# Kernel optimization log

Hardware: AMD Instinct MI355X
Metric: run time of the kernel (lower is better)

The kernel has to match this reference:

```python
import jax, jax.numpy as jnp
import numpy as np

N = 4096

def _backsub(rel_bounds):
    # rel_bounds: list; first entry is ((n,1),(n,1)) input bounds, rest are
    # (out, in+1) relative-bound matrices. Returns exact abs bounds (n,1).
    cur_lb, cur_ub = rel_bounds[-1]
    for prev_lb, prev_ub in reversed(rel_bounds[:-1]):
        bias_row = jnp.zeros((1, prev_lb.shape[-1]), prev_lb.dtype).at[0, -1].set(1.0)
        plb = jnp.concatenate([prev_lb, bias_row], axis=0)
        pub = jnp.concatenate([prev_ub, bias_row], axis=0)
        wp, wn = jax.nn.relu(cur_lb), jax.nn.relu(-cur_lb)
        new_lb = wp @ plb - wn @ pub
        wp, wn = jax.nn.relu(cur_ub), jax.nn.relu(-cur_ub)
        new_ub = wp @ pub - wn @ plb
        cur_lb, cur_ub = new_lb, new_ub
    return cur_lb, cur_ub


def setup_inputs() -> dict:
    key = jax.random.key(0)
    k = jax.random.split(key, 7)
    base = jax.random.normal(k[0], (N, 1), jnp.float32)
    eps = 0.1
    lb0 = base - eps
    ub0 = base + eps
    scale = 0.02  # keep bound magnitudes realistic through the matmul chain
    W1_lb = jax.random.normal(k[1], (N, N + 1), jnp.float32) * scale
    W1_ub = W1_lb + jnp.abs(jax.random.normal(k[2], (N, N + 1), jnp.float32)) * 0.001
    W2_lb = jax.random.normal(k[3], (N, N + 1), jnp.float32) * scale
    W2_ub = W2_lb + jnp.abs(jax.random.normal(k[4], (N, N + 1), jnp.float32)) * 0.001
    alphas = jax.random.uniform(k[5], (N,), jnp.float32)
    return {"lb0": lb0, "ub0": ub0, "W1_lb": W1_lb, "W1_ub": W1_ub,
            "W2_lb": W2_lb, "W2_ub": W2_ub, "alphas": alphas}


def reference(lb0, ub0, W1_lb, W1_ub, W2_lb, W2_ub, alphas):
    prev_lb, prev_ub = _backsub([(lb0, ub0), (W1_lb, W1_ub), (W2_lb, W2_ub)])  # (N,1)
    lb_s = prev_lb[:, 0]
    ub_s = prev_ub[:, 0]
    n = lb_s.shape[0]
    dt = prev_lb.dtype

    alpha = jnp.clip(alphas, 0.0, 1.0)
    alpha = jnp.where(lb_s > 0.0, jnp.ones((), dt), alpha)
    alpha = jnp.where(ub_s <= 0.0, jnp.zeros((), dt), alpha)
    current_lb = jnp.concatenate([jnp.diag(alpha), jnp.zeros((n, 1), dt)], axis=1)

    feps = jnp.finfo(dt).eps
    slope_ub = prev_ub / (prev_ub - prev_lb + feps)          # (N,1)
    slope_ub = jnp.where(prev_lb > 0.0, jnp.ones((), dt), slope_ub)
    slope_ub = jnp.where(prev_ub < 0.0, jnp.zeros((), dt), slope_ub)
    bias_ub = -prev_lb * slope_ub
    bias_ub = jnp.where((prev_lb > 0.0) | (prev_ub < 0.0), jnp.zeros((), dt), bias_ub)
    current_ub = jnp.concatenate([jnp.diag(slope_ub[:, 0]), bias_ub], axis=1)

    # stacked rel_bound appended by the layer: [0]=lower, [1]=upper, each (N, N+1)
    return jnp.stack([current_lb, current_ub])
```

## Files before the change

### kernel.cpp

```cpp
#include <hip/hip_runtime.h>
#include <float.h>

#define N4K 4096
#define NP1 4097

typedef __attribute__((ext_vector_type(4))) float f32x4;
typedef __attribute__((ext_vector_type(16))) float f32x16;
typedef __attribute__((ext_vector_type(8))) short bf16x8;

__device__ __forceinline__ unsigned short f2bf(float x) {
    union { float f; unsigned int u; } v; v.f = x;
    unsigned int r = v.u + 0x7FFFu + ((v.u >> 16) & 1u);
    return (unsigned short)(r >> 16);
}

__device__ __forceinline__ void gload_lds16(const void* g, void* l) {
    __builtin_amdgcn_global_load_lds(
        (const __attribute__((address_space(1))) unsigned int*)g,
        (__attribute__((address_space(3))) unsigned int*)l,
        16, 0, 0);
}

__device__ __forceinline__ void bar() {
    asm volatile("" ::: "memory");
    __builtin_amdgcn_s_barrier();
    asm volatile("" ::: "memory");
}

__global__ __launch_bounds__(256) void prep_A2(const float* __restrict__ W2lb,
                                               const float* __restrict__ W2ub,
                                               const float* __restrict__ mb,
                                               const float* __restrict__ db,
                                               unsigned short* __restrict__ Abf,
                                               float* __restrict__ bias_part) {
    int b = blockIdx.x;
    int chain = b >> 12, i = b & 4095;
    const float* row = (chain ? W2ub : W2lb) + (long long)i * NP1;
    unsigned short* abf_row = Abf + ((long long)chain << 24) + (long long)i * N4K;
    float s = chain ? 1.f : -1.f;
    float part = 0.f;
#pragma unroll 4
    for (int p = 0; p < 16; ++p) {
        int k = threadIdx.x + p * 256;
        float wv = row[k];
        abf_row[k] = f2bf(wv);
        part += wv * mb[k] + s * db[k] * fabsf(wv);
    }
    __shared__ float red[4];
#pragma unroll
    for (int off = 32; off; off >>= 1) part += __shfl_down(part, off);
    if ((threadIdx.x & 63) == 0) red[threadIdx.x >> 6] = part;
    __syncthreads();
    if (threadIdx.x == 0)
        bias_part[b] = red[0] + red[1] + red[2] + red[3] + row[4096];
}

__global__ __launch_bounds__(256) void prep_B(const float* __restrict__ W1lb,
                                              const float* __restrict__ W1ub,
                                              unsigned short* __restrict__ Bmt,
                                              unsigned short* __restrict__ Bdt) {
    __shared__ unsigned short Lm[64 * 65];
    __shared__ unsigned short Ld[64 * 65];
    int j0 = blockIdx.x * 64, k0 = blockIdx.y * 64;
    int t = threadIdx.x;
    int jj = t & 63, kkb = t >> 6;
#pragma unroll 4
    for (int p = 0; p < 16; ++p) {
        int kk = kkb + p * 4;
        long long off = (long long)(k0 + kk) * NP1 + j0 + jj;
        float l = W1lb[off], u = W1ub[off];
        Lm[kk * 65 + jj] = f2bf(0.5f * (l + u));
        Ld[kk * 65 + jj] = f2bf(0.5f * (u - l));
    }
    __syncthreads();
#pragma unroll
    for (int p = 0; p < 2; ++p) {
        int jl = p * 32 + (t >> 3);
        int kl = (t & 7) * 8;
        bf16x8 vm, vd;
#pragma unroll
        for (int i = 0; i < 8; ++i) {
            vm[i] = (short)Lm[(kl + i) * 65 + jl];
            vd[i] = (short)Ld[(kl + i) * 65 + jl];
        }
        *(bf16x8*)&Bmt[(long long)(j0 + jl) * N4K + k0 + kl] = vm;
        *(bf16x8*)&Bdt[(long long)(j0 + jl) * N4K + k0 + kl] = vd;
    }
}

__global__ __launch_bounds__(256) void prep_mbdb(const float* __restrict__ W1lb,
                                                 const float* __restrict__ W1ub,
                                                 float* __restrict__ mb,
                                                 float* __restrict__ db) {
    int k = blockIdx.x * 256 + threadIdx.x;
    if (k < N4K) {
        float l = W1lb[(long long)k * NP1 + 4096];
        float u = W1ub[(long long)k * NP1 + 4096];
        mb[k] = 0.5f * (l + u);
        db[k] = 0.5f * (u - l);
    }
}

__global__ __launch_bounds__(256)
void gemm_fused(const unsigned short* __restrict__ Abf,
                const unsigned short* __restrict__ Bmt,
                const unsigned short* __restrict__ Bdt,
                const float* __restrict__ lb0,
                const float* __restrict__ ub0,
                float* __restrict__ pp) {
    __shared__ unsigned short As[3][4096];
    __shared__ unsigned short Bms[3][4096];
    __shared__ unsigned short Bds[3][4096];

    int wg = blockIdx.x;
    int swz = (wg & 7) * 256 + (wg >> 3);
    int rt = swz & 63;
    int ct = swz >> 6;

    int chain = rt >> 5;
    const unsigned short* Aptr = Abf + ((long long)chain << 24) + (long long)(rt & 31) * 128 * N4K;
    const unsigned short* Bmp = Bmt + (long long)ct * 128 * N4K;
    const unsigned short* Bdp = Bdt + (long long)ct * 128 * N4K;

    int tid = threadIdx.x;
    int lane = tid & 63, w = tid >> 6;
    int wr = w >> 1, wc = w & 1;
    int la32 = lane & 31, kg = lane >> 5;

    int sr = tid >> 2;
    int sce = ((tid & 3) ^ ((sr >> 1) & 3)) << 3;
    const unsigned short* aB = Aptr + (long long)sr * N4K + sce;
    const unsigned short* mB = Bmp + (long long)sr * N4K + sce;
    const unsigned short* dB = Bdp + (long long)sr * N4K + sce;
    const long long R64 = 64LL * N4K;
    unsigned w512 = w * 512;

    f32x16 acc[2][2];
#pragma unroll
    for (int m = 0; m < 2; ++m)
#pragma unroll
        for (int n = 0; n < 2; ++n) acc[m][n] = (f32x16)(0.f);

#define STAGE(slot, koff)                                              \
    do {                                                               \
        gload_lds16(aB + (koff), &As[slot][w512]);                     \
        gload_lds16(aB + R64 + (koff), &As[slot][2048 + w512]);        \
        gload_lds16(mB + (koff), &Bms[slot][w512]);                    \
        gload_lds16(mB + R64 + (koff), &Bms[slot][2048 + w512]);       \
        gload_lds16(dB + (koff), &Bds[slot][w512]);                    \
        gload_lds16(dB + R64 + (koff), &Bds[slot][2048 + w512]);       \
    } while (0)

    STAGE(0, 0);
    STAGE(1, 32);
    asm volatile("s_waitcnt vmcnt(6)" ::: "memory");
    bar();

#define FRAG(arr, s, r, ks) \
    (*(const bf16x8*)&arr[s][(r) * 32 + (((2 * (ks) + kg) ^ (((r) >> 1) & 3)) * 8)])

    int cs = 0, st = 2;
#pragma unroll 1
    for (int t = 0; t < 128; ++t) {
        const bool pf = (t + 2 < 128);
        const long long koff = (long long)(t + 2) * 32;

        bf16x8 a[2][2], bm[2][2], bd[2][2];

#pragma unroll
        for (int m = 0; m < 2; ++m)
#pragma unroll
            for (int ks = 0; ks < 2; ++ks)
                a[m][ks] = FRAG(As, cs, wr * 64 + m * 32 + la32, ks);
#pragma unroll
        for (int n = 0; n < 2; ++n)
#pragma unroll
            for (int ks = 0; ks < 2; ++ks)
                bm[n][ks] = FRAG(Bms, cs, wc * 64 + n * 32 + la32, ks);
        if (pf) {
            gload_lds16(aB + koff, &As[st][w512]);
            gload_lds16(aB + R64 + koff, &As[st][2048 + w512]);
            gload_lds16(mB + koff, &Bms[st][w512]);
        }
        bar();
        asm volatile("s_waitcnt lgkmcnt(0)" ::: "memory");
        __builtin_amdgcn_s_setprio(1);
#pragma unroll
        for (int ks = 0; ks < 2; ++ks)
#pragma unroll
            for (int m = 0; m < 2; ++m)
#pragma unroll
                for (int n = 0; n < 2; ++n)
                    acc[m][n] = __builtin_amdgcn_mfma_f32_32x32x16_bf16(a[m][ks], bm[n][ks], acc[m][n], 0, 0, 0);
        __builtin_amdgcn_s_setprio(0);
        bar();

#pragma unroll
        for (int n = 0; n < 2; ++n)
#pragma unroll
            for (int ks = 0; ks < 2; ++ks)
                bd[n][ks] = FRAG(Bds, cs, wc * 64 + n * 32 + la32, ks);
        if (pf) {
            gload_lds16(mB + R64 + koff, &Bms[st][2048 + w512]);
            gload_lds16(dB + koff, &Bds[st][w512]);
            gload_lds16(dB + R64 + koff, &Bds[st][2048 + w512]);
        }
        bar();
        asm volatile("s_waitcnt lgkmcnt(0)" ::: "memory");
        __builtin_amdgcn_s_setprio(1);
#pragma unroll
        for (int ks = 0; ks < 2; ++ks)
#pragma unroll
            for (int m = 0; m < 2; ++m) {
                bf16x8 ax = chain ? (a[m][ks] & (short)0x7FFF) : (a[m][ks] | (short)0x8000);
#pragma unroll
                for (int n = 0; n < 2; ++n)
                    acc[m][n] = __builtin_amdgcn_mfma_f32_32x32x16_bf16(ax, bd[n][ks], acc[m][n], 0, 0, 0);
            }
        __builtin_amdgcn_s_setprio(0);

        if (pf) asm volatile("s_waitcnt vmcnt(6)" ::: "memory");
        else    asm volatile("s_waitcnt vmcnt(0)" ::: "memory");
        bar();

        cs = (cs == 2) ? 0 : cs + 1;
        st = (st == 2) ? 0 : st + 1;
    }
#undef FRAG
#undef STAGE

    float s = chain ? 1.f : -1.f;
    float rowpart[2][16];
#pragma unroll
    for (int m = 0; m < 2; ++m)
#pragma unroll
        for (int r = 0; r < 16; ++r) rowpart[m][r] = 0.f;

    int jbase = ct * 128 + wc * 64;
#pragma unroll
    for (int n = 0; n < 2; ++n) {
        int j = jbase + n * 32 + la32;
        float l0 = lb0[j], u0 = ub0[j];
        float mj = 0.5f * (l0 + u0);
        float sdj = s * 0.5f * (u0 - l0);
#pragma unroll
        for (int m = 0; m < 2; ++m)
#pragma unroll
            for (int r = 0; r < 16; ++r) {
                float v = acc[m][n][r];
                rowpart[m][r] += v * mj + sdj * fabsf(v);
            }
    }
    long long rowg = (long long)chain * N4K + (rt & 31) * 128 + wr * 64;
    long long slice = (long long)(ct * 2 + wc) * 8192;
    int hi4 = kg * 4;
#pragma unroll
    for (int m = 0; m < 2; ++m)
#pragma unroll
        for (int r = 0; r < 16; ++r) {
            float v = rowpart[m][r];
            v += __shfl_xor(v, 1);
            v += __shfl_xor(v, 2);
            v += __shfl_xor(v, 4);
            v += __shfl_xor(v, 8);
            v += __shfl_xor(v, 16);
            if (la32 == 0)
                pp[slice + rowg + m * 32 + (r & 3) + 8 * (r >> 2) + hi4] = v;
        }
}

__global__ __launch_bounds__(256) void reduce_pp(const float* __restrict__ pp,
                                                 const float* __restrict__ bias_part,
                                                 float* __restrict__ prev) {
    int j = blockIdx.x * 256 + threadIdx.x;
    float s = bias_part[j];
#pragma unroll 8
    for (int c = 0; c < 64; ++c) s += pp[(long long)c * 8192 + j];
    prev[j] = s;
}

__global__ __launch_bounds__(256) void epilogue(const float* __restrict__ prev,
                                                const float* __restrict__ alphas,
                                                float* __restrict__ out) {
    int i = blockIdx.x * 256 + threadIdx.x;
    if (i >= N4K) return;
    float lb = prev[i], ub = prev[N4K + i];
    float a = fminf(fmaxf(alphas[i], 0.f), 1.f);
    if (lb > 0.f) a = 1.f;
    if (ub <= 0.f) a = 0.f;
    float slope = ub / (ub - lb + FLT_EPSILON);
    if (lb > 0.f) slope = 1.f;
    if (ub < 0.f) slope = 0.f;
    float bias = -lb * slope;
    if (lb > 0.f || ub < 0.f) bias = 0.f;
    long long P = NP1, half = (long long)N4K * NP1;
    out[(long long)i * P + i] = a;
    out[half + (long long)i * P + i] = slope;
    out[half + (long long)i * P + 4096] = bias;
}

extern "C" void kernel_launch(void* const* d_in, const int* in_sizes, int n_in,
                              void* d_out, int out_size, void* d_ws, size_t ws_size,
                              hipStream_t stream) {
    const float* lb0    = (const float*)d_in[0];
    const float* ub0    = (const float*)d_in[1];
    const float* W1lb   = (const float*)d_in[2];
    const float* W1ub   = (const float*)d_in[3];
    const float* W2lb   = (const float*)d_in[4];
    const float* W2ub   = (const float*)d_in[5];
    const float* alphas = (const float*)d_in[6];

    char* ws = (char*)d_ws;
    float* bias_part = (float*)ws;
    float* mb   = (float*)(ws + 32768);
    float* db   = (float*)(ws + 49152);
    float* prev = (float*)(ws + 32768);
    unsigned short* Abf = (unsigned short*)(ws + 65536);
    unsigned short* Bmt = (unsigned short*)(ws + 65536 + 67108864);
    unsigned short* Bdt = (unsigned short*)(ws + 65536 + 100663296);
    size_t need = 65536ULL + 67108864ULL + 2ULL * 33554432ULL;
    if (ws_size < need) return;

    float* pp = (float*)d_out;

    (void)hipMemsetAsync(d_out, 0, (size_t)out_size * 4, stream);

    prep_mbdb<<<16, 256, 0, stream>>>(W1lb, W1ub, mb, db);
    prep_A2<<<8192, 256, 0, stream>>>(W2lb, W2ub, mb, db, Abf, bias_part);
    prep_B<<<dim3(64, 64), 256, 0, stream>>>(W1lb, W1ub, Bmt, Bdt);
    gemm_fused<<<2048, 256, 0, stream>>>(Abf, Bmt, Bdt, lb0, ub0, pp);
    reduce_pp<<<32, 256, 0, stream>>>(pp, bias_part, prev);
    (void)hipMemsetAsync(d_out, 0, 64 * 8192 * 4, stream);
    epilogue<<<16, 256, 0, stream>>>(prev, alphas, (float*)d_out);
}
```

Measured before the change: 760.8 us.

## Halve K-tile to 16 and merge the two compute phases per iteration

Shrinks the K step of the fused GEMM from 32 to 16, which halves the LDS buffers, and runs twice as many iterations. Each iteration now loads all A, Bm and Bd fragments at once and interleaves the two MFMA chains. This removes the intra-iteration barriers and lgkmcnt waits of the two-phase split. The smaller LDS footprint may allow higher occupancy, but per-iteration sync and loop overhead double relative to the MFMA work, and each tile issues shorter load bursts.

Result: slower. 970.6 us (+27.6%).

```diff
diff --git a/kernel.cpp b/kernel.cpp
--- a/kernel.cpp
+++ b/kernel.cpp
@@ -108,9 +108,9 @@
                 const float* __restrict__ lb0,
                 const float* __restrict__ ub0,
                 float* __restrict__ pp) {
-    __shared__ unsigned short As[3][4096];
-    __shared__ unsigned short Bms[3][4096];
-    __shared__ unsigned short Bds[3][4096];
+    __shared__ unsigned short As[3][2048];
+    __shared__ unsigned short Bms[3][2048];
+    __shared__ unsigned short Bds[3][2048];
 
     int wg = blockIdx.x;
     int swz = (wg & 7) * 256 + (wg >> 3);
@@ -127,12 +127,11 @@
     int wr = w >> 1, wc = w & 1;
     int la32 = lane & 31, kg = lane >> 5;
 
-    int sr = tid >> 2;
-    int sce = ((tid & 3) ^ ((sr >> 1) & 3)) << 3;
+    int sr = tid >> 1;
+    int sce = ((tid & 1) ^ ((sr >> 2) & 1)) << 3;
     const unsigned short* aB = Aptr + (long long)sr * N4K + sce;
     const unsigned short* mB = Bmp + (long long)sr * N4K + sce;
     const unsigned short* dB = Bdp + (long long)sr * N4K + sce;
-    const long long R64 = 64LL * N4K;
     unsigned w512 = w * 512;
 
     f32x16 acc[2][2];
@@ -141,85 +140,53 @@
 #pragma unroll
         for (int n = 0; n < 2; ++n) acc[m][n] = (f32x16)(0.f);
 
-#define STAGE(slot, koff)                                              \
-    do {                                                               \
-        gload_lds16(aB + (koff), &As[slot][w512]);                     \
-        gload_lds16(aB + R64 + (koff), &As[slot][2048 + w512]);        \
-        gload_lds16(mB + (koff), &Bms[slot][w512]);                    \
-        gload_lds16(mB + R64 + (koff), &Bms[slot][2048 + w512]);       \
-        gload_lds16(dB + (koff), &Bds[slot][w512]);                    \
-        gload_lds16(dB + R64 + (koff), &Bds[slot][2048 + w512]);       \
+#define STAGE(slot, koff)                             \
+    do {                                              \
+        gload_lds16(aB + (koff), &As[slot][w512]);    \
+        gload_lds16(mB + (koff), &Bms[slot][w512]);   \
+        gload_lds16(dB + (koff), &Bds[slot][w512]);   \
     } while (0)
 
     STAGE(0, 0);
-    STAGE(1, 32);
-    asm volatile("s_waitcnt vmcnt(6)" ::: "memory");
+    STAGE(1, 16);
+    asm volatile("s_waitcnt vmcnt(3)" ::: "memory");
     bar();
 
-#define FRAG(arr, s, r, ks) \
-    (*(const bf16x8*)&arr[s][(r) * 32 + (((2 * (ks) + kg) ^ (((r) >> 1) & 3)) * 8)])
+#define FRAG(arr, s, r) \
+    (*(const bf16x8*)&arr[s][(r) * 16 + (((kg ^ (((r) >> 2) & 1))) * 8)])
 
     int cs = 0, st = 2;
 #pragma unroll 1
-    for (int t = 0; t < 128; ++t) {
-        const bool pf = (t + 2 < 128);
-        const long long koff = (long long)(t + 2) * 32;
-
-        bf16x8 a[2][2], bm[2][2], bd[2][2];
-
-#pragma unroll
-        for (int m = 0; m < 2; ++m)
-#pragma unroll
-            for (int ks = 0; ks < 2; ++ks)
-                a[m][ks] = FRAG(As, cs, wr * 64 + m * 32 + la32, ks);
-#pragma unroll
-        for (int n = 0; n < 2; ++n)
-#pragma unroll
-            for (int ks = 0; ks < 2; ++ks)
-                bm[n][ks] = FRAG(Bms, cs, wc * 64 + n * 32 + la32, ks);
+    for (int t = 0; t < 256; ++t) {
+        const bool pf = (t + 2 < 256);
+        const long long koff = (long long)(t + 2) * 16;
+
+        bf16x8 a[2], bm[2], bd[2];
+#pragma unroll
+        for (int m = 0; m < 2; ++m) a[m] = FRAG(As, cs, wr * 64 + m * 32 + la32);
+#pragma unroll
+        for (int n = 0; n < 2; ++n) {
+            bm[n] = FRAG(Bms, cs, wc * 64 + n * 32 + la32);
+            bd[n] = FRAG(Bds, cs, wc * 64 + n * 32 + la32);
+        }
         if (pf) {
             gload_lds16(aB + koff, &As[st][w512]);
-            gload_lds16(aB + R64 + koff, &As[st][2048 + w512]);
             gload_lds16(mB + koff, &Bms[st][w512]);
-        }
-        bar();
-        asm volatile("s_waitcnt lgkmcnt(0)" ::: "memory");
+            gload_lds16(dB + koff, &Bds[st][w512]);
+        }
         __builtin_amdgcn_s_setprio(1);
 #pragma unroll
-        for (int ks = 0; ks < 2; ++ks)
-#pragma unroll
-            for (int m = 0; m < 2; ++m)
-#pragma unroll
-                for (int n = 0; n < 2; ++n)
-                    acc[m][n] = __builtin_amdgcn_mfma_f32_32x32x16_bf16(a[m][ks], bm[n][ks], acc[m][n], 0, 0, 0);
+        for (int m = 0; m < 2; ++m) {
+            bf16x8 ax = chain ? (a[m] & (short)0x7FFF) : (a[m] | (short)0x8000);
+#pragma unroll
+            for (int n = 0; n < 2; ++n) {
+                acc[m][n] = __builtin_amdgcn_mfma_f32_32x32x16_bf16(a[m], bm[n], acc[m][n], 0, 0, 0);
+                acc[m][n] = __builtin_amdgcn_mfma_f32_32x32x16_bf16(ax, bd[n], acc[m][n], 0, 0, 0);
+            }
+        }
         __builtin_amdgcn_s_setprio(0);
-        bar();
-
-#pragma unroll
-        for (int n = 0; n < 2; ++n)
-#pragma unroll
-            for (int ks = 0; ks < 2; ++ks)
-                bd[n][ks] = FRAG(Bds, cs, wc * 64 + n * 32 + la32, ks);
-        if (pf) {
-            gload_lds16(mB + R64 + koff, &Bms[st][2048 + w512]);
-            gload_lds16(dB + koff, &Bds[st][w512]);
-            gload_lds16(dB + R64 + koff, &Bds[st][2048 + w512]);
-        }
-        bar();
-        asm volatile("s_waitcnt lgkmcnt(0)" ::: "memory");
-        __builtin_amdgcn_s_setprio(1);
-#pragma unroll
-        for (int ks = 0; ks < 2; ++ks)
-#pragma unroll
-            for (int m = 0; m < 2; ++m) {
-                bf16x8 ax = chain ? (a[m][ks] & (short)0x7FFF) : (a[m][ks] | (short)0x8000);
-#pragma unroll
-                for (int n = 0; n < 2; ++n)
-                    acc[m][n] = __builtin_amdgcn_mfma_f32_32x32x16_bf16(ax, bd[n][ks], acc[m][n], 0, 0, 0);
-            }
-        __builtin_amdgcn_s_setprio(0);
-
-        if (pf) asm volatile("s_waitcnt vmcnt(6)" ::: "memory");
+
+        if (pf) asm volatile("s_waitcnt vmcnt(3)" ::: "memory");
         else    asm volatile("s_waitcnt vmcnt(0)" ::: "memory");
         bar();
 
```
